# Kernel tuning notes

Hardware: AMD Instinct MI355X
Metric: run time of the kernel (lower is better)

## Reference

```python
import jax, jax.numpy as jnp
import numpy as np

H, D, DIM = 8, 128, 1024   # heads, dim_head, model dim (inner_dim = H*D = DIM)
QB, N = 16, 512            # 'q' and 'n' dims of the [q, n, dim] inputs


def layer_norm(x, g, b, eps=1e-5):
    mu = x.mean(-1, keepdims=True)
    var = ((x - mu) ** 2).mean(-1, keepdims=True)
    return (x - mu) / jnp.sqrt(var + eps) * g + b


def setup_inputs() -> dict:
    key = jax.random.key(0)
    ks = jax.random.split(key, 8)
    rn = lambda k, shape, s=1.0: jax.random.normal(k, shape, jnp.float32) * s
    return {
        'q': rn(ks[0], (QB, N, DIM)),
        'k': rn(ks[1], (QB, N, DIM)),
        'v': rn(ks[2], (QB, N, DIM)),
        'ln_g': jnp.ones(DIM, jnp.float32),
        'ln_b': jnp.zeros(DIM, jnp.float32),
        'w_in': rn(ks[3], (H * D, DIM), 0.02),          # Linear(dim -> inner_dim), no bias
        'wp_w1': rn(ks[4], (D, 2 * D), 0.05),           # weight_predictor Linear(2d -> d)
        'wp_b1': jnp.zeros(D, jnp.float32),
        'wp_ln_g': jnp.ones(D, jnp.float32),
        'wp_ln_b': jnp.zeros(D, jnp.float32),
        'wp_w2': rn(ks[5], (3, D), 0.05),               # Linear(d -> 3)
        'wp_b2': jnp.zeros(3, jnp.float32),
        'w_out': rn(ks[6], (DIM, H * D), 0.02),         # output Linear(inner_dim -> dim)
        'b_out': jnp.zeros(DIM, jnp.float32),
    }


def reference(q, k, v, ln_g, ln_b, w_in, wp_w1, wp_b1, wp_ln_g, wp_ln_b,
              wp_w2, wp_b2, w_out, b_out):
    def proj(t):
        x = layer_norm(t, ln_g, ln_b) @ w_in.T                 # [Q, N, H*D]
        Qd, Nd = t.shape[0], t.shape[1]
        return x.reshape(Qd, Nd, H, D).transpose(2, 0, 1, 3)   # [h, q, n, d]

    f_q, f_k, f_v = proj(q), proj(k), proj(v)

    # cosine similarity component
    dots = jnp.einsum('hqnd,hqmd->hqnm', f_q, f_k)
    qn = jnp.linalg.norm(f_q, axis=-1)                          # [h, q, n]
    kn = jnp.linalg.norm(f_k, axis=-1)                          # [h, q, m]
    cosine_sim = dots / (qn[..., :, None] * kn[..., None, :])

    q_centered = f_q - f_q.mean(-1, keepdims=True)

    # variance component (unbiased variance, clipped ratio vs target_var=1)
    q_var = jnp.var(f_q, axis=-1, ddof=1)
    k_var = jnp.var(f_k, axis=-1, ddof=1)
    q_ratio = 2.0 * jnp.minimum(q_var, 1.0) / (q_var + 1.0)
    k_ratio = 2.0 * jnp.minimum(k_var, 1.0) / (k_var + 1.0)
    var_component = jnp.einsum('hqn,hqm->hqnm', q_ratio, k_ratio)

    # decorrelation-scaled covariance component (overwrites the dead loop in the source)
    q_flat = q_centered.reshape(H, -1, D)                        # [h, q*n, d]
    feat_corr = jnp.einsum('hnd,hne->hde', q_flat, q_flat) / q_flat.shape[1]
    feat_corr = feat_corr * (1.0 - jnp.eye(D, dtype=feat_corr.dtype))
    decorr_score = jnp.linalg.norm(feat_corr, axis=(-2, -1)) / (D * D)
    decorr_scale = jnp.exp(-5.0 * decorr_score)[:, None, None, None]
    cov_component = cosine_sim * decorr_scale

    # dynamic per-head weight mixing
    q_global = f_q.mean(axis=(1, 2))                             # [h, d]
    k_global = f_k.mean(axis=(1, 2))
    feats = jnp.concatenate([q_global, k_global], axis=-1)       # [h, 2d]
    h1 = jnp.maximum(layer_norm(feats @ wp_w1.T + wp_b1, wp_ln_g, wp_ln_b), 0.0)
    weights = jax.nn.softmax(h1 @ wp_w2.T + wp_b2, axis=-1)      # [h, 3]
    cw = weights[:, 0][:, None, None, None]
    vw = weights[:, 1][:, None, None, None]
    ww = weights[:, 2][:, None, None, None]
    mixed = cw * cosine_sim + vw * cov_component + ww * var_component

    out = jnp.einsum('hqnm,hqmd->hqnd', mixed, f_v)
    out = out.transpose(1, 2, 0, 3).reshape(q.shape[0], q.shape[1], H * D)
    return out @ w_out.T + b_out
```

## Files before the change

kernel.cpp:

```cpp
#include <hip/hip_runtime.h>
#include <hip/hip_bf16.h>

typedef unsigned short u16;
typedef __attribute__((ext_vector_type(8))) short short8;
typedef __attribute__((ext_vector_type(4))) float floatx4;

#define H 8
#define D 128
#define DIM 1024
#define QB 16
#define NSEQ 512
#define R 8192

__device__ inline u16 f2b(float x) {
    union { float f; unsigned int u; } c{x};
    unsigned int lsb = (c.u >> 16) & 1;
    unsigned int r = c.u + 0x7fffu + lsb;
    return (u16)(r >> 16);
}
__device__ inline float b2f(u16 u) {
    union { unsigned int i; float f; } c;
    c.i = (unsigned int)u << 16;
    return c.f;
}

#define GLOAD_LDS16(gptr, lptr)                                                        \
    __builtin_amdgcn_global_load_lds(                                                  \
        (const __attribute__((address_space(1))) unsigned int*)(gptr),                 \
        (__attribute__((address_space(3))) unsigned int*)(lptr), 16, 0, 0)

__global__ __launch_bounds__(256) void prep(const float* __restrict__ q,
                                            const float* __restrict__ k,
                                            const float* __restrict__ v,
                                            const float* __restrict__ g,
                                            const float* __restrict__ b,
                                            u16* __restrict__ out,
                                            const float* __restrict__ w_in,
                                            const float* __restrict__ w_out,
                                            u16* __restrict__ w_in16,
                                            u16* __restrict__ w_out16) {
    const int bb = blockIdx.x;
    const int tid = threadIdx.x;
    if (bb < 2048) {
        const int n4each = DIM * DIM / 4;
        int i = bb * 256 + tid;
        const float* src; u16* dst; int j;
        if (i < n4each) { src = w_in;  dst = w_in16;  j = i; }
        else            { src = w_out; dst = w_out16; j = i - n4each; }
        float4 vv = *(const float4*)(src + (size_t)j * 4);
        ushort4 pk;
        pk.x = f2b(vv.x); pk.y = f2b(vv.y); pk.z = f2b(vv.z); pk.w = f2b(vv.w);
        *(ushort4*)(dst + (size_t)j * 4) = pk;
        return;
    }
    const int b2 = bb - 2048;
    const int wv = tid >> 6, lane = tid & 63;
    const int row = b2 * 4 + wv;
    const int y = row >> 13, r = row & 8191;
    const float* src = (y == 0) ? q : (y == 1) ? k : v;
    const float* rp = src + (size_t)r * DIM;
    float4 x0 = *(const float4*)(rp + (0 * 64 + lane) * 4);
    float4 x1 = *(const float4*)(rp + (1 * 64 + lane) * 4);
    float4 x2 = *(const float4*)(rp + (2 * 64 + lane) * 4);
    float4 x3 = *(const float4*)(rp + (3 * 64 + lane) * 4);
    float sum = (x0.x + x0.y + x0.z + x0.w) + (x1.x + x1.y + x1.z + x1.w)
              + (x2.x + x2.y + x2.z + x2.w) + (x3.x + x3.y + x3.z + x3.w);
    float sq = x0.x*x0.x + x0.y*x0.y + x0.z*x0.z + x0.w*x0.w
             + x1.x*x1.x + x1.y*x1.y + x1.z*x1.z + x1.w*x1.w
             + x2.x*x2.x + x2.y*x2.y + x2.z*x2.z + x2.w*x2.w
             + x3.x*x3.x + x3.y*x3.y + x3.z*x3.z + x3.w*x3.w;
#pragma unroll
    for (int o = 32; o > 0; o >>= 1) {
        sum += __shfl_xor(sum, o);
        sq  += __shfl_xor(sq, o);
    }
    float mean = sum * (1.0f / DIM);
    float var = sq * (1.0f / DIM) - mean * mean;
    float rstd = rsqrtf(var + 1e-5f);
    u16* op = out + ((size_t)y * R + r) * DIM;
    float4 xs[4] = {x0, x1, x2, x3};
#pragma unroll
    for (int p = 0; p < 4; p++) {
        int e4 = (p * 64 + lane) * 4;
        float4 gv = *(const float4*)(g + e4);
        float4 bv = *(const float4*)(b + e4);
        ushort4 pk;
        pk.x = f2b((xs[p].x - mean) * rstd * gv.x + bv.x);
        pk.y = f2b((xs[p].y - mean) * rstd * gv.y + bv.y);
        pk.z = f2b((xs[p].z - mean) * rstd * gv.z + bv.z);
        pk.w = f2b((xs[p].w - mean) * rstd * gv.w + bv.w);
        *(ushort4*)(op + e4) = pk;
    }
}

__global__ __launch_bounds__(256) void gemm_qkv(const u16* __restrict__ A,
                                                const u16* __restrict__ B,
                                                u16* __restrict__ qT,
                                                u16* __restrict__ fqb,
                                                u16* __restrict__ kTh,
                                                u16* __restrict__ vT,
                                                float* __restrict__ qn,
                                                float* __restrict__ qm,
                                                float* __restrict__ qr,
                                                float* __restrict__ kn,
                                                float* __restrict__ kr) {
    __shared__ __align__(16) u16 smem[19712];
    u16* As  = smem;
    u16* Bs  = smem + 4096;
    u16* As2 = smem + 8192;
    u16* Bs2 = smem + 12288;
    float* sred = (float*)(smem + 18432);
    float* invb = (float*)(smem + 19456);

    const int tid = threadIdx.x;
    const int bb = blockIdx.x;
    const int xcd = bb & 7, j0 = bb >> 3;
    const int h = j0 & 7;
    const int rowblk = xcd * 24 + (j0 >> 3);
    const int m0 = rowblk * 128, n0 = h * 128;
    const int seg = rowblk >> 6;
    const int lrb = (rowblk & 63) * 128;

    const int wave = tid >> 6, lane = tid & 63;
    const int wm = (wave >> 1) * 64, wn = (wave & 1) * 64;
    const int fr = lane & 15, kq = lane >> 4;
    const int srow = tid >> 2, scol = (tid & 3) * 8;

    floatx4 acc[4][4] = {};
    const size_t aOff0 = (size_t)(m0 + srow) * DIM + scol;
    const size_t aOff1 = (size_t)(m0 + 64 + srow) * DIM + scol;
    const size_t bOff0 = (size_t)(n0 + srow) * DIM + scol;
    const size_t bOff1 = (size_t)(n0 + 64 + srow) * DIM + scol;

    for (int kt = 0; kt < DIM; kt += 64) {
        GLOAD_LDS16(A + aOff0 + kt, As + tid * 8);
        GLOAD_LDS16(A + aOff1 + kt, As + (256 + tid) * 8);
        GLOAD_LDS16(B + bOff0 + kt, Bs + tid * 8);
        GLOAD_LDS16(B + bOff1 + kt, Bs + (256 + tid) * 8);
        GLOAD_LDS16(A + aOff0 + kt + 32, As2 + tid * 8);
        GLOAD_LDS16(A + aOff1 + kt + 32, As2 + (256 + tid) * 8);
        GLOAD_LDS16(B + bOff0 + kt + 32, Bs2 + tid * 8);
        GLOAD_LDS16(B + bOff1 + kt + 32, Bs2 + (256 + tid) * 8);
        __syncthreads();
        short8 xf[4], wf[4];
#pragma unroll
        for (int i = 0; i < 4; i++)
            xf[i] = *(const short8*)&As[(wm + i * 16 + fr) * 32 + kq * 8];
#pragma unroll
        for (int j = 0; j < 4; j++)
            wf[j] = *(const short8*)&Bs[(wn + j * 16 + fr) * 32 + kq * 8];
#pragma unroll
        for (int j = 0; j < 4; j++)
#pragma unroll
            for (int i = 0; i < 4; i++)
                acc[j][i] = __builtin_amdgcn_mfma_f32_16x16x32_bf16(wf[j], xf[i], acc[j][i], 0, 0, 0);
        short8 xg[4], wg[4];
#pragma unroll
        for (int i = 0; i < 4; i++)
            xg[i] = *(const short8*)&As2[(wm + i * 16 + fr) * 32 + kq * 8];
#pragma unroll
        for (int j = 0; j < 4; j++)
            wg[j] = *(const short8*)&Bs2[(wn + j * 16 + fr) * 32 + kq * 8];
#pragma unroll
        for (int j = 0; j < 4; j++)
#pragma unroll
            for (int i = 0; i < 4; i++)
                acc[j][i] = __builtin_amdgcn_mfma_f32_16x16x32_bf16(wg[j], xg[i], acc[j][i], 0, 0, 0);
        __syncthreads();
    }

    if (seg <= 1) {
        const int half = wn >> 6;
#pragma unroll
        for (int i = 0; i < 4; i++) {
            float s = 0.0f, qs = 0.0f;
#pragma unroll
            for (int j = 0; j < 4; j++)
#pragma unroll
                for (int rg = 0; rg < 4; rg++) {
                    float vv = acc[j][i][rg];
                    s += vv; qs += vv * vv;
                }
            s += __shfl_xor(s, 16); qs += __shfl_xor(qs, 16);
            s += __shfl_xor(s, 32); qs += __shfl_xor(qs, 32);
            if (kq == 0) {
                int rl = wm + i * 16 + fr;
                sred[rl * 4 + half * 2 + 0] = s;
                sred[rl * 4 + half * 2 + 1] = qs;
            }
        }
        __syncthreads();
        if (tid < 128) {
            float sum = sred[tid * 4 + 0] + sred[tid * 4 + 2];
            float sq  = sred[tid * 4 + 1] + sred[tid * 4 + 3];
            float nrm = sqrtf(sq);
            float var = (sq - sum * sum * (1.0f / D)) * (1.0f / (D - 1));
            float ratio = 2.0f * fminf(var, 1.0f) / (var + 1.0f);
            size_t idx = (size_t)h * R + lrb + tid;
            if (seg == 0) {
                qn[idx] = nrm; qm[idx] = sum * (1.0f / D); qr[idx] = ratio;
            } else {
                kn[idx] = nrm; kr[idx] = ratio;
                invb[tid] = 1.0f / nrm;
            }
        }
        __syncthreads();
    }

    u16* dstT = (seg == 0) ? qT : (seg == 1) ? kTh : vT;
#pragma unroll
    for (int i = 0; i < 4; i++) {
        const int rl = wm + i * 16 + fr;
        const float sc = (seg == 1) ? invb[rl] : 1.0f;
#pragma unroll
        for (int j = 0; j < 4; j++) {
#pragma unroll
            for (int rg = 0; rg < 4; rg++) {
                const int cl = wn + j * 16 + kq * 4 + rg;
                dstT[(size_t)(h * D + cl) * R + lrb + rl] = f2b(acc[j][i][rg] * sc);
            }
        }
    }

    if (seg == 0) {
        __syncthreads();
        u16* Tw = smem + wave * 4608;
#pragma unroll
        for (int i = 0; i < 4; i++)
#pragma unroll
            for (int j = 0; j < 4; j++) {
                ushort4 pk;
                pk.x = f2b(acc[j][i][0]); pk.y = f2b(acc[j][i][1]);
                pk.z = f2b(acc[j][i][2]); pk.w = f2b(acc[j][i][3]);
                *(ushort4*)&Tw[(i * 16 + fr) * 72 + j * 16 + kq * 4] = pk;
            }
        __syncthreads();
#pragma unroll
        for (int p = 0; p < 16; p++) {
            int rloc = p * 4 + kq;
            int c4 = fr * 4;
            ushort4 v = *(const ushort4*)&Tw[rloc * 72 + c4];
            *(ushort4*)&fqb[(size_t)(lrb + wm + rloc) * DIM + h * D + wn + c4] = v;
        }
    }
}

__global__ __launch_bounds__(256) void fanout(const u16* __restrict__ qT,
                                              const u16* __restrict__ kTh,
                                              const u16* __restrict__ vT,
                                              const float* __restrict__ qm,
                                              const float* __restrict__ kn,
                                              const float* __restrict__ kr,
                                              float* __restrict__ qg,
                                              float* __restrict__ kg,
                                              float* __restrict__ ubuf,
                                              float* __restrict__ s2,
                                              float* __restrict__ P,
                                              u16* __restrict__ Mt,
                                              float* __restrict__ sv) {
    __shared__ __align__(16) u16 sm[17040];
    u16* As = sm;
    u16* Bs = sm + 8192;
    float* wbuf  = (float*)(sm + 16384);
    float* svred = (float*)(sm + 16512);
    float* redS  = (float*)(sm + 17024);

    const int bb = blockIdx.x;
    const int tid = threadIdx.x;
    const int wave = tid >> 6, lane = tid & 63;
    const int wm = (wave >> 1) * 64, wn = (wave & 1) * 64;
    const int fr = lane & 15, kq = lane >> 4;
    const int srow = tid >> 2, scol = (tid & 3) * 8;

    if (bb < 128) {
        const int qi = bb & 15, h = bb >> 4;
        const int m0g = qi * 512;
        const size_t a0 = (size_t)(h * D + srow) * R + m0g + scol;
        const size_t a1 = (size_t)(h * D + 64 + srow) * R + m0g + scol;
        const int e_id = tid & 127, mb16 = (tid >> 7) * 16;
        float svacc = 0.0f;
        floatx4 acc[4][4] = {};
        for (int kt = 0; kt < 512; kt += 64) {
#pragma unroll
            for (int kc = 0; kc < 2; kc++) {
                GLOAD_LDS16(vT + a0 + kt + kc * 32, As + kc * 4096 + tid * 8);
                GLOAD_LDS16(vT + a1 + kt + kc * 32, As + kc * 4096 + (256 + tid) * 8);
                GLOAD_LDS16(kTh + a0 + kt + kc * 32, Bs + kc * 4096 + tid * 8);
                GLOAD_LDS16(kTh + a1 + kt + kc * 32, Bs + kc * 4096 + (256 + tid) * 8);
            }
            if (tid < 64) wbuf[tid] = kr[(size_t)h * R + m0g + kt + tid];
            __syncthreads();
#pragma unroll
            for (int kc = 0; kc < 2; kc++) {
                short8 af[4], bf[4];
#pragma unroll
                for (int i = 0; i < 4; i++)
                    af[i] = *(const short8*)&As[kc * 4096 + (wm + i * 16 + fr) * 32 + kq * 8];
#pragma unroll
                for (int j = 0; j < 4; j++)
                    bf[j] = *(const short8*)&Bs[kc * 4096 + (wn + j * 16 + fr) * 32 + kq * 8];
#pragma unroll
                for (int i = 0; i < 4; i++)
#pragma unroll
                    for (int j = 0; j < 4; j++)
                        acc[i][j] = __builtin_amdgcn_mfma_f32_16x16x32_bf16(af[i], bf[j], acc[i][j], 0, 0, 0);
                short8 va = *(const short8*)&As[kc * 4096 + e_id * 32 + mb16];
                short8 vb = *(const short8*)&As[kc * 4096 + e_id * 32 + mb16 + 8];
#pragma unroll
                for (int jm = 0; jm < 8; jm++)
                    svacc += b2f((u16)va[jm]) * wbuf[kc * 32 + mb16 + jm];
#pragma unroll
                for (int jm = 0; jm < 8; jm++)
                    svacc += b2f((u16)vb[jm]) * wbuf[kc * 32 + mb16 + 8 + jm];
            }
            __syncthreads();
        }
        u16* mb = Mt + (size_t)(h * QB + qi) * D * D;
#pragma unroll
        for (int i = 0; i < 4; i++) {
            int er = wm + i * 16 + kq * 4;
#pragma unroll
            for (int j = 0; j < 4; j++) {
                int dc = wn + j * 16 + fr;
#pragma unroll
                for (int r = 0; r < 4; r++)
                    mb[(size_t)(er + r) * D + dc] = f2b(acc[i][j][r]);
            }
        }
        svred[tid] = svacc;
        __syncthreads();
        if (tid < 128)
            sv[(size_t)(h * QB + qi) * D + tid] = svred[tid] + svred[tid + 128];
    } else if (bb < 192) {
        const int t = bb - 128;
        const int c = t & 7, h = t >> 3;
        floatx4 acc[4][4] = {};
        const size_t a0 = (size_t)(h * D + srow) * R + c * 1024 + scol;
        const size_t a1 = (size_t)(h * D + 64 + srow) * R + c * 1024 + scol;
        for (int kt = 0; kt < 1024; kt += 64) {
#pragma unroll
            for (int kc = 0; kc < 2; kc++) {
                GLOAD_LDS16(qT + a0 + kt + kc * 32, As + kc * 4096 + tid * 8);
                GLOAD_LDS16(qT + a1 + kt + kc * 32, As + kc * 4096 + (256 + tid) * 8);
            }
            __syncthreads();
#pragma unroll
            for (int kc = 0; kc < 2; kc++) {
                short8 af[4], bf[4];
#pragma unroll
                for (int i = 0; i < 4; i++)
                    af[i] = *(const short8*)&As[kc * 4096 + (wm + i * 16 + fr) * 32 + kq * 8];
#pragma unroll
                for (int j = 0; j < 4; j++)
                    bf[j] = *(const short8*)&As[kc * 4096 + (wn + j * 16 + fr) * 32 + kq * 8];
#pragma unroll
                for (int i = 0; i < 4; i++)
#pragma unroll
                    for (int j = 0; j < 4; j++)
                        acc[i][j] = __builtin_amdgcn_mfma_f32_16x16x32_bf16(af[i], bf[j], acc[i][j], 0, 0, 0);
            }
            __syncthreads();
        }
        float* base = P + (size_t)(h * 8 + c) * (D * D);
#pragma unroll
        for (int i = 0; i < 4; i++) {
            int dr = wm + i * 16 + kq * 4;
#pragma unroll
            for (int j = 0; j < 4; j++) {
                int ec = wn + j * 16 + fr;
                float4 f4;
                f4.x = acc[i][j][0]; f4.y = acc[i][j][1];
                f4.z = acc[i][j][2]; f4.w = acc[i][j][3];
                *(float4*)&base[(size_t)ec * D + dr] = f4;
            }
        }
    } else {
        const int t = bb - 192;
        const int dg = t & 15, h = (t >> 4) & 7, mode = t >> 7;
        const u16* fT = mode ? kTh : qT;
        const float* wvec = mode ? kn : qm;
        const int wv = tid >> 6;
        float (*red)[4] = (float(*)[4])redS;
        const float* wp = wvec + (size_t)h * R;
        for (int dd = 0; dd < 8; dd++) {
            int d = dg * 8 + dd;
            const u16* rowp = fT + (size_t)(h * D + d) * R;
            float s = 0.0f, su = 0.0f;
            for (int it = 0; it < 8; it++) {
                int r = it * 1024 + tid * 4;
                uint2 pv = *(const uint2*)(rowp + r);
                float4 w = *(const float4*)(wp + r);
                float v0 = b2f((u16)(pv.x & 0xffffu)), v1 = b2f((u16)(pv.x >> 16));
                float v2 = b2f((u16)(pv.y & 0xffffu)), v3 = b2f((u16)(pv.y >> 16));
                if (mode) s += v0 * w.x + v1 * w.y + v2 * w.z + v3 * w.w;
                else {
                    s += v0 + v1 + v2 + v3;
                    su += v0 * w.x + v1 * w.y + v2 * w.z + v3 * w.w;
                }
            }
#pragma unroll
            for (int o = 32; o > 0; o >>= 1) {
                s += __shfl_xor(s, o);
                su += __shfl_xor(su, o);
            }
            if ((tid & 63) == 0) { red[0][wv] = s; red[1][wv] = su; }
            __syncthreads();
            if (tid == 0) {
                float S  = red[0][0] + red[0][1] + red[0][2] + red[0][3];
                float SU = red[1][0] + red[1][1] + red[1][2] + red[1][3];
                if (mode) kg[h * D + d] = S * (1.0f / R);
                else { qg[h * D + d] = S * (1.0f / R); ubuf[h * D + d] = SU; }
            }
            __syncthreads();
        }
        if (!mode && dg == 0) {
            float tt = 0.0f;
            for (int it = 0; it < 8; it++) {
                float4 m4 = *(const float4*)(qm + (size_t)h * R + it * 1024 + tid * 4);
                tt += m4.x * m4.x + m4.y * m4.y + m4.z * m4.z + m4.w * m4.w;
            }
#pragma unroll
            for (int o = 32; o > 0; o >>= 1) tt += __shfl_xor(tt, o);
            if ((tid & 63) == 0) red[0][wv] = tt;
            __syncthreads();
            if (tid == 0) s2[h] = red[0][0] + red[0][1] + red[0][2] + red[0][3];
        }
    }
}

__global__ __launch_bounds__(256) void attn2(const u16* __restrict__ fqb,
                                             const u16* __restrict__ Mt,
                                             const float* __restrict__ qn,
                                             const float* __restrict__ qr,
                                             const float* __restrict__ sv,
                                             const float* __restrict__ P,
                                             const float* __restrict__ ubuf,
                                             const float* __restrict__ s2b,
                                             const float* __restrict__ qg,
                                             const float* __restrict__ kg,
                                             const float* __restrict__ w1,
                                             const float* __restrict__ b1,
                                             const float* __restrict__ lng,
                                             const float* __restrict__ lnb,
                                             const float* __restrict__ w2,
                                             const float* __restrict__ b2,
                                             u16* __restrict__ outb) {
    __shared__ u16 As[128 * 128];
    __shared__ u16 Bs[128 * 128];
    __shared__ float hscratch[1024];
    const int nb = blockIdx.x, qi = blockIdx.y, h = blockIdx.z;
    const int tid = threadIdx.x;
    const int wave = tid >> 6, lane = tid & 63;
    const int wm = (wave >> 1) * 64, wn = (wave & 1) * 64;
    const int fr = lane & 15, kq = lane >> 4;
    const int srow = tid >> 2, scol = (tid & 3) * 8;
    const int n0g = qi * 512 + nb * 128;
    const size_t a0 = (size_t)(n0g + srow) * DIM + h * D + scol;
    const size_t a1 = (size_t)(n0g + 64 + srow) * DIM + h * D + scol;
    const u16* mtb = Mt + (size_t)(h * QB + qi) * D * D;

#pragma unroll
    for (int kc = 0; kc < 4; kc++) {
        GLOAD_LDS16(fqb + a0 + kc * 32, As + kc * 4096 + tid * 8);
        GLOAD_LDS16(fqb + a1 + kc * 32, As + kc * 4096 + (256 + tid) * 8);
        GLOAD_LDS16(mtb + (size_t)srow * D + kc * 32 + scol, Bs + kc * 4096 + tid * 8);
        GLOAD_LDS16(mtb + (size_t)(64 + srow) * D + kc * 32 + scol, Bs + kc * 4096 + (256 + tid) * 8);
    }

    float c0, c1;
    {
        float s2h = s2b[h];
        float part = 0.0f;
        for (int k = 0; k < 64; k++) {
            int de = k * 256 + tid;
            int dd = de >> 7, ee = de & 127;
            float gsum = 0.0f;
#pragma unroll
            for (int c = 0; c < 8; c++)
                gsum += P[(size_t)(h * 8 + c) * (D * D) + de];
            if (dd != ee) {
                float vv = (gsum - ubuf[h * D + dd] - ubuf[h * D + ee] + s2h) * (1.0f / R);
                part += vv * vv;
            }
        }
#pragma unroll
        for (int o = 32; o > 0; o >>= 1) part += __shfl_xor(part, o);
        if (lane == 0) hscratch[wave] = part;
        __syncthreads();
        float Ssum = hscratch[0] + hscratch[1] + hscratch[2] + hscratch[3];
        float dscale = expf(-5.0f * sqrtf(Ssum) / (float)(D * D));
        __syncthreads();

        float* hs1 = hscratch;
        float* hs2 = hscratch + 256;
        float* hs3 = hscratch + 512;
        float* hfe = hscratch + 768;
        hfe[tid] = (tid < 128) ? qg[h * D + tid] : kg[h * D + tid - 128];
        __syncthreads();
        float yv = 0.0f;
        if (tid < 128) {
            float a = b1[tid];
            for (int i = 0; i < 256; i++) a = fmaf(hfe[i], w1[tid * 256 + i], a);
            yv = a;
        }
        hs1[tid] = (tid < 128) ? yv : 0.0f;
        hs2[tid] = (tid < 128) ? yv * yv : 0.0f;
        __syncthreads();
        for (int s = 128; s > 0; s >>= 1) {
            if (tid < s) { hs1[tid] += hs1[tid + s]; hs2[tid] += hs2[tid + s]; }
            __syncthreads();
        }
        float mean = hs1[0] * (1.0f / 128.0f);
        float var = hs2[0] * (1.0f / 128.0f) - mean * mean;
        float rstd = rsqrtf(var + 1e-5f);
        float rel = 0.0f;
        if (tid < 128)
            rel = fmaxf((yv - mean) * rstd * lng[tid] + lnb[tid], 0.0f);
        __syncthreads();
        hs1[tid] = (tid < 128) ? rel * w2[0 * 128 + tid] : 0.0f;
        hs2[tid] = (tid < 128) ? rel * w2[1 * 128 + tid] : 0.0f;
        hs3[tid] = (tid < 128) ? rel * w2[2 * 128 + tid] : 0.0f;
        __syncthreads();
        for (int s = 128; s > 0; s >>= 1) {
            if (tid < s) { hs1[tid] += hs1[tid + s]; hs2[tid] += hs2[tid + s]; hs3[tid] += hs3[tid + s]; }
            __syncthreads();
        }
        if (tid == 0) {
            float g0 = hs1[0] + b2[0], g1 = hs2[0] + b2[1], g2 = hs3[0] + b2[2];
            float mx = fmaxf(g0, fmaxf(g1, g2));
            float e0 = expf(g0 - mx), e1 = expf(g1 - mx), e2 = expf(g2 - mx);
            float inv = 1.0f / (e0 + e1 + e2);
            hs1[0] = e0 * inv + e1 * inv * dscale;
            hs1[1] = e2 * inv;
        }
        __syncthreads();
        c0 = hs1[0]; c1 = hs1[1];
    }

    asm volatile("s_waitcnt vmcnt(0)" ::: "memory");
    __syncthreads();

    floatx4 acc[4][4] = {};
#pragma unroll
    for (int kc = 0; kc < 4; kc++) {
        short8 af[4], bf[4];
#pragma unroll
        for (int i = 0; i < 4; i++)
            af[i] = *(const short8*)&As[kc * 4096 + (wm + i * 16 + fr) * 32 + kq * 8];
#pragma unroll
        for (int j = 0; j < 4; j++)
            bf[j] = *(const short8*)&Bs[kc * 4096 + (wn + j * 16 + fr) * 32 + kq * 8];
#pragma unroll
        for (int i = 0; i < 4; i++)
#pragma unroll
            for (int j = 0; j < 4; j++)
                acc[i][j] = __builtin_amdgcn_mfma_f32_16x16x32_bf16(af[i], bf[j], acc[i][j], 0, 0, 0);
    }
#pragma unroll
    for (int i = 0; i < 4; i++) {
        int nr = n0g + wm + i * 16 + kq * 4;
        float4 nv = *(const float4*)&qn[(size_t)h * R + nr];
        float4 rv = *(const float4*)&qr[(size_t)h * R + nr];
        float sc1[4] = {c0 / nv.x, c0 / nv.y, c0 / nv.z, c0 / nv.w};
        float sc2[4] = {c1 * rv.x, c1 * rv.y, c1 * rv.z, c1 * rv.w};
#pragma unroll
        for (int j = 0; j < 4; j++) {
            int ec = wn + j * 16 + fr;
            float svv = sv[(size_t)(h * QB + qi) * D + ec];
#pragma unroll
            for (int r = 0; r < 4; r++)
                outb[(size_t)(nr + r) * DIM + h * D + ec] = f2b(sc1[r] * acc[i][j][r] + sc2[r] * svv);
        }
    }
}

__global__ __launch_bounds__(256) void gemm_out(const u16* __restrict__ A,
                                                const u16* __restrict__ B,
                                                const float* __restrict__ bias,
                                                float* __restrict__ C) {
    __shared__ u16 As[128 * 64];
    __shared__ u16 Bs[128 * 64];
    const int tid = threadIdx.x;
    const int bb = blockIdx.x;
    const int xcd = bb & 7, jj = bb >> 3;
    const int col = jj & 7, rowblk = xcd * 8 + (jj >> 3);
    const int m0 = rowblk * 128, n0 = col * 128;
    const int wave = tid >> 6, lane = tid & 63;
    const int wm = (wave >> 1) * 64, wn = (wave & 1) * 64;
    const int fr = lane & 15, kq = lane >> 4;
    const int srow = tid >> 2, scol = (tid & 3) * 8;
    floatx4 acc[4][4] = {};
    const size_t aOff0 = (size_t)(m0 + srow) * DIM + scol;
    const size_t aOff1 = (size_t)(m0 + 64 + srow) * DIM + scol;
    const size_t bOff0 = (size_t)(n0 + srow) * DIM + scol;
    const size_t bOff1 = (size_t)(n0 + 64 + srow) * DIM + scol;
    for (int kt = 0; kt < DIM; kt += 64) {
        GLOAD_LDS16(A + aOff0 + kt, As + tid * 8);
        GLOAD_LDS16(A + aOff1 + kt, As + (256 + tid) * 8);
        GLOAD_LDS16(A + aOff0 + kt + 32, As + (512 + tid) * 8);
        GLOAD_LDS16(A + aOff1 + kt + 32, As + (768 + tid) * 8);
        GLOAD_LDS16(B + bOff0 + kt, Bs + tid * 8);
        GLOAD_LDS16(B + bOff1 + kt, Bs + (256 + tid) * 8);
        GLOAD_LDS16(B + bOff0 + kt + 32, Bs + (512 + tid) * 8);
        GLOAD_LDS16(B + bOff1 + kt + 32, Bs + (768 + tid) * 8);
        __syncthreads();
        short8 af[4], bf[4];
#pragma unroll
        for (int i = 0; i < 4; i++)
            af[i] = *(const short8*)&As[(wm + i * 16 + fr) * 32 + kq * 8];
#pragma unroll
        for (int j = 0; j < 4; j++)
            bf[j] = *(const short8*)&Bs[(wn + j * 16 + fr) * 32 + kq * 8];
#pragma unroll
        for (int i = 0; i < 4; i++)
#pragma unroll
            for (int j = 0; j < 4; j++)
                acc[i][j] = __builtin_amdgcn_mfma_f32_16x16x32_bf16(af[i], bf[j], acc[i][j], 0, 0, 0);
        short8 ag[4], bg[4];
#pragma unroll
        for (int i = 0; i < 4; i++)
            ag[i] = *(const short8*)&As[4096 + (wm + i * 16 + fr) * 32 + kq * 8];
#pragma unroll
        for (int j = 0; j < 4; j++)
            bg[j] = *(const short8*)&Bs[4096 + (wn + j * 16 + fr) * 32 + kq * 8];
#pragma unroll
        for (int i = 0; i < 4; i++)
#pragma unroll
            for (int j = 0; j < 4; j++)
                acc[i][j] = __builtin_amdgcn_mfma_f32_16x16x32_bf16(ag[i], bg[j], acc[i][j], 0, 0, 0);
        __syncthreads();
    }
#pragma unroll
    for (int i = 0; i < 4; i++) {
        int rbase = m0 + wm + i * 16 + kq * 4;
#pragma unroll
        for (int j = 0; j < 4; j++) {
            int c = n0 + wn + j * 16 + fr;
            float badd = bias[c];
#pragma unroll
            for (int r = 0; r < 4; r++)
                C[(size_t)(rbase + r) * DIM + c] = acc[i][j][r] + badd;
        }
    }
}

extern "C" void kernel_launch(void* const* d_in, const int* in_sizes, int n_in,
                              void* d_out, int out_size, void* d_ws, size_t ws_size,
                              hipStream_t stream) {
    (void)in_sizes; (void)n_in; (void)out_size; (void)ws_size;
    const float* q      = (const float*)d_in[0];
    const float* k      = (const float*)d_in[1];
    const float* v      = (const float*)d_in[2];
    const float* ln_g   = (const float*)d_in[3];
    const float* ln_b   = (const float*)d_in[4];
    const float* w_in   = (const float*)d_in[5];
    const float* wp_w1  = (const float*)d_in[6];
    const float* wp_b1  = (const float*)d_in[7];
    const float* wp_lng = (const float*)d_in[8];
    const float* wp_lnb = (const float*)d_in[9];
    const float* wp_w2  = (const float*)d_in[10];
    const float* wp_b2  = (const float*)d_in[11];
    const float* w_out  = (const float*)d_in[12];
    const float* b_out  = (const float*)d_in[13];
    float* out = (float*)d_out;

    constexpr size_t F = (size_t)R * DIM;
    u16* lnall   = (u16*)d_ws;
    u16* fqb     = lnall + 3 * F;
    u16* qT      = fqb + F;
    u16* kTh     = qT + F;
    u16* vT      = kTh + F;
    u16* w_in16  = vT + F;
    u16* w_out16 = w_in16 + (size_t)DIM * DIM;
    u16* Mt      = w_out16 + (size_t)DIM * DIM;
    float* P     = (float*)(Mt + (size_t)H * QB * D * D);
    float* qn    = P + (size_t)32 * H * D * D;
    float* qm    = qn + (size_t)H * R;
    float* qr    = qm + (size_t)H * R;
    float* kn    = qr + (size_t)H * R;
    float* kr    = kn + (size_t)H * R;
    float* qg    = kr + (size_t)H * R;
    float* kg    = qg + H * D;
    float* ubuf  = kg + H * D;
    float* s2    = ubuf + H * D;
    float* Spart = s2 + H;
    float* coef  = Spart + H * 8;
    float* svb   = coef + 16;

    prep<<<8192, 256, 0, stream>>>(q, k, v, ln_g, ln_b, lnall,
                                   w_in, w_out, w_in16, w_out16);

    gemm_qkv<<<1536, 256, 0, stream>>>(lnall, w_in16, qT, fqb, kTh, vT,
                                       qn, qm, qr, kn, kr);

    fanout<<<448, 256, 0, stream>>>(qT, kTh, vT, qm, kn, kr,
                                    qg, kg, ubuf, s2, P, Mt, svb);

    attn2<<<dim3(4, QB, H), 256, 0, stream>>>(fqb, Mt, qn, qr, svb,
                                              P, ubuf, s2, qg, kg,
                                              wp_w1, wp_b1, wp_lng, wp_lnb,
                                              wp_w2, wp_b2, lnall);

    gemm_out<<<512, 256, 0, stream>>>(lnall, w_out16, b_out, out);
}
```

Measured before the change: 333.8 us.

## Compute per-head mixing coefficients once in fanout's last block per head

Moves the decorrelation-score and weight-predictor MLP computation out of every attention block into a single last-arriving block per head in the fanout kernel. A per-head atomic counter, reset by an extra prep block, elects that block. The attention kernel then just reads two precomputed coefficients. This removes redundant reads of the P partial correlation buffers and repeated small MLPs across 512 blocks, at the cost of a serialized tail in fanout and reliance on atomic/threadfence ordering.

```diff
diff --git a/kernel.cpp b/kernel.cpp
--- a/kernel.cpp
+++ b/kernel.cpp
@@ -38,9 +38,14 @@
                                             const float* __restrict__ w_in,
                                             const float* __restrict__ w_out,
                                             u16* __restrict__ w_in16,
-                                            u16* __restrict__ w_out16) {
+                                            u16* __restrict__ w_out16,
+                                            unsigned int* __restrict__ cnt) {
     const int bb = blockIdx.x;
     const int tid = threadIdx.x;
+    if (bb >= 8192) {
+        if (tid < H) cnt[tid] = 0u;
+        return;
+    }
     if (bb < 2048) {
         const int n4each = DIM * DIM / 4;
         int i = bb * 256 + tid;
@@ -257,13 +262,22 @@
                                               float* __restrict__ s2,
                                               float* __restrict__ P,
                                               u16* __restrict__ Mt,
-                                              float* __restrict__ sv) {
+                                              float* __restrict__ sv,
+                                              const float* __restrict__ w1,
+                                              const float* __restrict__ b1,
+                                              const float* __restrict__ lng,
+                                              const float* __restrict__ lnb,
+                                              const float* __restrict__ w2,
+                                              const float* __restrict__ b2,
+                                              float* __restrict__ coef,
+                                              unsigned int* __restrict__ cnt) {
     __shared__ __align__(16) u16 sm[17040];
     u16* As = sm;
     u16* Bs = sm + 8192;
     float* wbuf  = (float*)(sm + 16384);
     float* svred = (float*)(sm + 16512);
     float* redS  = (float*)(sm + 17024);
+    __shared__ unsigned int lastflag;
 
     const int bb = blockIdx.x;
     const int tid = threadIdx.x;
@@ -272,6 +286,7 @@
     const int fr = lane & 15, kq = lane >> 4;
     const int srow = tid >> 2, scol = (tid & 3) * 8;
 
+    int myh = -1;
     if (bb < 128) {
         const int qi = bb & 15, h = bb >> 4;
         const int m0g = qi * 512;
@@ -334,6 +349,7 @@
     } else if (bb < 192) {
         const int t = bb - 128;
         const int c = t & 7, h = t >> 3;
+        myh = h;
         floatx4 acc[4][4] = {};
         const size_t a0 = (size_t)(h * D + srow) * R + c * 1024 + scol;
         const size_t a1 = (size_t)(h * D + 64 + srow) * R + c * 1024 + scol;
@@ -377,6 +393,7 @@
     } else {
         const int t = bb - 192;
         const int dg = t & 15, h = (t >> 4) & 7, mode = t >> 7;
+        myh = h;
         const u16* fT = mode ? kTh : qT;
         const float* wvec = mode ? kn : qm;
         const int wv = tid >> 6;
@@ -426,28 +443,90 @@
             if (tid == 0) s2[h] = red[0][0] + red[0][1] + red[0][2] + red[0][3];
         }
     }
+
+    if (myh >= 0) {
+        __syncthreads();
+        __threadfence();
+        if (tid == 0) lastflag = atomicAdd(&cnt[myh], 1u);
+        __syncthreads();
+        if (lastflag == 39u) {
+            __threadfence();
+            float s2h = s2[myh];
+            float part = 0.0f;
+            for (int kk = 0; kk < 64; kk++) {
+                int de = kk * 256 + tid;
+                int dd = de >> 7, ee = de & 127;
+                float gsum = 0.0f;
+#pragma unroll
+                for (int c = 0; c < 8; c++)
+                    gsum += P[(size_t)(myh * 8 + c) * (D * D) + de];
+                if (dd != ee) {
+                    float vv = (gsum - ubuf[myh * D + dd] - ubuf[myh * D + ee] + s2h) * (1.0f / R);
+                    part += vv * vv;
+                }
+            }
+#pragma unroll
+            for (int o = 32; o > 0; o >>= 1) part += __shfl_xor(part, o);
+            float* hs1 = (float*)sm;
+            float* hs2 = hs1 + 256;
+            float* hs3 = hs2 + 256;
+            float* hfe = hs3 + 256;
+            if ((tid & 63) == 0) hs1[tid >> 6] = part;
+            __syncthreads();
+            float Ssum = hs1[0] + hs1[1] + hs1[2] + hs1[3];
+            float dscale = expf(-5.0f * sqrtf(Ssum) / (float)(D * D));
+            __syncthreads();
+            hfe[tid] = (tid < 128) ? qg[myh * D + tid] : kg[myh * D + tid - 128];
+            __syncthreads();
+            float yv = 0.0f;
+            if (tid < 128) {
+                float a = b1[tid];
+                for (int i = 0; i < 256; i++) a = fmaf(hfe[i], w1[tid * 256 + i], a);
+                yv = a;
+            }
+            hs1[tid] = (tid < 128) ? yv : 0.0f;
+            hs2[tid] = (tid < 128) ? yv * yv : 0.0f;
+            __syncthreads();
+            for (int s = 128; s > 0; s >>= 1) {
+                if (tid < s) { hs1[tid] += hs1[tid + s]; hs2[tid] += hs2[tid + s]; }
+                __syncthreads();
+            }
+            float mean = hs1[0] * (1.0f / 128.0f);
+            float var = hs2[0] * (1.0f / 128.0f) - mean * mean;
+            float rstd = rsqrtf(var + 1e-5f);
+            float rel = 0.0f;
+            if (tid < 128)
+                rel = fmaxf((yv - mean) * rstd * lng[tid] + lnb[tid], 0.0f);
+            __syncthreads();
+            hs1[tid] = (tid < 128) ? rel * w2[0 * 128 + tid] : 0.0f;
+            hs2[tid] = (tid < 128) ? rel * w2[1 * 128 + tid] : 0.0f;
+            hs3[tid] = (tid < 128) ? rel * w2[2 * 128 + tid] : 0.0f;
+            __syncthreads();
+            for (int s = 128; s > 0; s >>= 1) {
+                if (tid < s) { hs1[tid] += hs1[tid + s]; hs2[tid] += hs2[tid + s]; hs3[tid] += hs3[tid + s]; }
+                __syncthreads();
+            }
+            if (tid == 0) {
+                float g0 = hs1[0] + b2[0], g1 = hs2[0] + b2[1], g2 = hs3[0] + b2[2];
+                float mx = fmaxf(g0, fmaxf(g1, g2));
+                float e0 = expf(g0 - mx), e1 = expf(g1 - mx), e2 = expf(g2 - mx);
+                float inv = 1.0f / (e0 + e1 + e2);
+                coef[myh * 2 + 0] = e0 * inv + e1 * inv * dscale;
+                coef[myh * 2 + 1] = e2 * inv;
+            }
+        }
+    }
 }
 
-__global__ __launch_bounds__(256) void attn2(const u16* __restrict__ fqb,
-                                             const u16* __restrict__ Mt,
-                                             const float* __restrict__ qn,
-                                             const float* __restrict__ qr,
-                                             const float* __restrict__ sv,
-                                             const float* __restrict__ P,
-                                             const float* __restrict__ ubuf,
-                                             const float* __restrict__ s2b,
-                                             const float* __restrict__ qg,
-                                             const float* __restrict__ kg,
-                                             const float* __restrict__ w1,
-                                             const float* __restrict__ b1,
-                                             const float* __restrict__ lng,
-                                             const float* __restrict__ lnb,
-                                             const float* __restrict__ w2,
-                                             const float* __restrict__ b2,
-                                             u16* __restrict__ outb) {
+__global__ __launch_bounds__(256) void attn_mfma(const u16* __restrict__ fqb,
+                                                 const u16* __restrict__ Mt,
+                                                 const float* __restrict__ qn,
+                                                 const float* __restrict__ qr,
+                                                 const float* __restrict__ sv,
+                                                 const float* __restrict__ coef,
+                                                 u16* __restrict__ outb) {
     __shared__ u16 As[128 * 128];
     __shared__ u16 Bs[128 * 128];
-    __shared__ float hscratch[1024];
     const int nb = blockIdx.x, qi = blockIdx.y, h = blockIdx.z;
     const int tid = threadIdx.x;
     const int wave = tid >> 6, lane = tid & 63;
@@ -458,7 +537,6 @@
     const size_t a0 = (size_t)(n0g + srow) * DIM + h * D + scol;
     const size_t a1 = (size_t)(n0g + 64 + srow) * DIM + h * D + scol;
     const u16* mtb = Mt + (size_t)(h * QB + qi) * D * D;
-
 #pragma unroll
     for (int kc = 0; kc < 4; kc++) {
         GLOAD_LDS16(fqb + a0 + kc * 32, As + kc * 4096 + tid * 8);
@@ -466,80 +544,7 @@
         GLOAD_LDS16(mtb + (size_t)srow * D + kc * 32 + scol, Bs + kc * 4096 + tid * 8);
         GLOAD_LDS16(mtb + (size_t)(64 + srow) * D + kc * 32 + scol, Bs + kc * 4096 + (256 + tid) * 8);
     }
-
-    float c0, c1;
-    {
-        float s2h = s2b[h];
-        float part = 0.0f;
-        for (int k = 0; k < 64; k++) {
-            int de = k * 256 + tid;
-            int dd = de >> 7, ee = de & 127;
-            float gsum = 0.0f;
-#pragma unroll
-            for (int c = 0; c < 8; c++)
-                gsum += P[(size_t)(h * 8 + c) * (D * D) + de];
-            if (dd != ee) {
-                float vv = (gsum - ubuf[h * D + dd] - ubuf[h * D + ee] + s2h) * (1.0f / R);
-                part += vv * vv;
-            }
-        }
-#pragma unroll
-        for (int o = 32; o > 0; o >>= 1) part += __shfl_xor(part, o);
-        if (lane == 0) hscratch[wave] = part;
-        __syncthreads();
-        float Ssum = hscratch[0] + hscratch[1] + hscratch[2] + hscratch[3];
-        float dscale = expf(-5.0f * sqrtf(Ssum) / (float)(D * D));
-        __syncthreads();
-
-        float* hs1 = hscratch;
-        float* hs2 = hscratch + 256;
-        float* hs3 = hscratch + 512;
-        float* hfe = hscratch + 768;
-        hfe[tid] = (tid < 128) ? qg[h * D + tid] : kg[h * D + tid - 128];
-        __syncthreads();
-        float yv = 0.0f;
-        if (tid < 128) {
-            float a = b1[tid];
-            for (int i = 0; i < 256; i++) a = fmaf(hfe[i], w1[tid * 256 + i], a);
-            yv = a;
-        }
-        hs1[tid] = (tid < 128) ? yv : 0.0f;
-        hs2[tid] = (tid < 128) ? yv * yv : 0.0f;
-        __syncthreads();
-        for (int s = 128; s > 0; s >>= 1) {
-            if (tid < s) { hs1[tid] += hs1[tid + s]; hs2[tid] += hs2[tid + s]; }
-            __syncthreads();
-        }
-        float mean = hs1[0] * (1.0f / 128.0f);
-        float var = hs2[0] * (1.0f / 128.0f) - mean * mean;
-        float rstd = rsqrtf(var + 1e-5f);
-        float rel = 0.0f;
-        if (tid < 128)
-            rel = fmaxf((yv - mean) * rstd * lng[tid] + lnb[tid], 0.0f);
-        __syncthreads();
-        hs1[tid] = (tid < 128) ? rel * w2[0 * 128 + tid] : 0.0f;
-        hs2[tid] = (tid < 128) ? rel * w2[1 * 128 + tid] : 0.0f;
-        hs3[tid] = (tid < 128) ? rel * w2[2 * 128 + tid] : 0.0f;
-        __syncthreads();
-        for (int s = 128; s > 0; s >>= 1) {
-            if (tid < s) { hs1[tid] += hs1[tid + s]; hs2[tid] += hs2[tid + s]; hs3[tid] += hs3[tid + s]; }
-            __syncthreads();
-        }
-        if (tid == 0) {
-            float g0 = hs1[0] + b2[0], g1 = hs2[0] + b2[1], g2 = hs3[0] + b2[2];
-            float mx = fmaxf(g0, fmaxf(g1, g2));
-            float e0 = expf(g0 - mx), e1 = expf(g1 - mx), e2 = expf(g2 - mx);
-            float inv = 1.0f / (e0 + e1 + e2);
-            hs1[0] = e0 * inv + e1 * inv * dscale;
-            hs1[1] = e2 * inv;
-        }
-        __syncthreads();
-        c0 = hs1[0]; c1 = hs1[1];
-    }
-
-    asm volatile("s_waitcnt vmcnt(0)" ::: "memory");
     __syncthreads();
-
     floatx4 acc[4][4] = {};
 #pragma unroll
     for (int kc = 0; kc < 4; kc++) {
@@ -556,6 +561,7 @@
             for (int j = 0; j < 4; j++)
                 acc[i][j] = __builtin_amdgcn_mfma_f32_16x16x32_bf16(af[i], bf[j], acc[i][j], 0, 0, 0);
     }
+    float c0 = coef[2 * h], c1 = coef[2 * h + 1];
 #pragma unroll
     for (int i = 0; i < 4; i++) {
         int nr = n0g + wm + i * 16 + kq * 4;
@@ -683,23 +689,22 @@
     float* kg    = qg + H * D;
     float* ubuf  = kg + H * D;
     float* s2    = ubuf + H * D;
-    float* Spart = s2 + H;
-    float* coef  = Spart + H * 8;
+    unsigned int* cnt = (unsigned int*)(s2 + H);
+    float* coef  = (float*)(cnt + H) + 8;
     float* svb   = coef + 16;
 
-    prep<<<8192, 256, 0, stream>>>(q, k, v, ln_g, ln_b, lnall,
-                                   w_in, w_out, w_in16, w_out16);
+    prep<<<8193, 256, 0, stream>>>(q, k, v, ln_g, ln_b, lnall,
+                                   w_in, w_out, w_in16, w_out16, cnt);
 
     gemm_qkv<<<1536, 256, 0, stream>>>(lnall, w_in16, qT, fqb, kTh, vT,
                                        qn, qm, qr, kn, kr);
 
     fanout<<<448, 256, 0, stream>>>(qT, kTh, vT, qm, kn, kr,
-                                    qg, kg, ubuf, s2, P, Mt, svb);
-
-    attn2<<<dim3(4, QB, H), 256, 0, stream>>>(fqb, Mt, qn, qr, svb,
-                                              P, ubuf, s2, qg, kg,
-                                              wp_w1, wp_b1, wp_lng, wp_lnb,
-                                              wp_w2, wp_b2, lnall);
+                                    qg, kg, ubuf, s2, P, Mt, svb,
+                                    wp_w1, wp_b1, wp_lng, wp_lnb,
+                                    wp_w2, wp_b2, coef, cnt);
+
+    attn_mfma<<<dim3(4, QB, H), 256, 0, stream>>>(fqb, Mt, qn, qr, svb, coef, lnall);
 
     gemm_out<<<512, 256, 0, stream>>>(lnall, w_out16, b_out, out);
 }
```

Result: slower. 361.7 us (+8.4%).
